# Performance work log

Hardware: AMD Instinct MI355X
Metric: run time of the kernel (lower is better)

## Reference

```python
import jax, jax.numpy as jnp
import numpy as np

B, N, D_IN, D_OUT = 64, 512, 128, 128
LEAKY_SLOPE = 0.2  # DGL GATConv default negative_slope


def setup_inputs() -> dict:
    key = jax.random.key(0)
    k1, k2, k3, k4, k5 = jax.random.split(key, 5)
    embedding = jax.random.normal(k1, (B, N, D_IN), dtype=jnp.float32)
    W = jax.random.normal(k2, (D_IN, D_OUT), dtype=jnp.float32) / np.sqrt(D_IN)
    attn_l = jax.random.normal(k3, (D_OUT,), dtype=jnp.float32) * 0.1
    attn_r = jax.random.normal(k4, (D_OUT,), dtype=jnp.float32) * 0.1
    bias = jax.random.normal(k5, (D_OUT,), dtype=jnp.float32) * 0.01
    return {"embedding": embedding, "W": W, "attn_l": attn_l, "attn_r": attn_r, "bias": bias}


def reference(embedding, W, attn_l, attn_r, bias):
    # --- constructure_graph: per-sample adjacency E @ E^T thresholded at its
    # scalar mean, plus self-loops. edge (i, j): src=i (row), dst=j (col).
    scores = jnp.einsum('bnd,bmd->bnm', embedding, embedding)        # [B,N,N]
    thresh = jnp.mean(scores, axis=(1, 2), keepdims=True)            # scalar per sample
    self_loop = jnp.eye(scores.shape[1], dtype=bool)                  # [N,N]
    mask = (scores > thresh) | self_loop                              # [B,src,dst]

    # --- GATConv (1 head, eval mode: feat_drop/attn_drop are identity)
    z = jnp.einsum('bnd,de->bne', embedding, W)                       # [B,N,D_OUT]
    el = z @ attn_l                                                   # [B,N] source term
    er = z @ attn_r                                                   # [B,N] dest term
    e = jax.nn.leaky_relu(el[:, :, None] + er[:, None, :], LEAKY_SLOPE)  # [B,src,dst]
    e = jnp.where(mask, e, -jnp.inf)
    alpha = jax.nn.softmax(e, axis=1)                                 # softmax over incoming (src) edges per dst
    h = jnp.einsum('bij,bid->bjd', alpha, z)                          # aggregate src -> dst
    h = jax.nn.elu(h + bias)                                          # bias + activation=F.elu

    # --- mean pool over nodes
    return jnp.mean(h, axis=1)                                        # [B, D_OUT]
```

## Files before the change

kernel.cpp:

```cpp
#include <hip/hip_runtime.h>
#include <math.h>

#define BATCH 64
#define NN 512
#define DD 128
#define SLOPE 0.2f

typedef unsigned short u16;
typedef short bf16x8 __attribute__((ext_vector_type(8)));
typedef u16 u16x4 __attribute__((ext_vector_type(4)));
typedef u16 u16x8 __attribute__((ext_vector_type(8)));
typedef float f32x4 __attribute__((ext_vector_type(4)));

static __device__ __forceinline__ u16 f2bf(float x) {
    unsigned int u = __float_as_uint(x);
    return (u16)((u + 0x7fffu + ((u >> 16) & 1u)) >> 16);
}
static __device__ __forceinline__ float bf2f(u16 h) {
    return __uint_as_float(((unsigned int)h) << 16);
}
static __device__ __forceinline__ void gld16(const u16* g, u16* lds) {
    __builtin_amdgcn_global_load_lds(
        (const __attribute__((address_space(1))) unsigned int*)g,
        (__attribute__((address_space(3))) unsigned int*)lds, 16, 0, 0);
}

__global__ __launch_bounds__(256) void k_prep(const float* __restrict__ W,
                                              const float* __restrict__ E,
                                              u16* __restrict__ WtHi,
                                              u16* __restrict__ WtLo,
                                              float* __restrict__ cs2,
                                              float* __restrict__ out) {
    __shared__ float csr[8][128];
    int t = threadIdx.x;
    if (blockIdx.x == 0) {
        int n = t & 127, half = t >> 7;
        #pragma unroll
        for (int g = 0; g < 8; ++g) {
            u16x8 hv, lv;
            #pragma unroll
            for (int j = 0; j < 8; ++j) {
                float v = W[(size_t)(half * 64 + g * 8 + j) * DD + n];
                u16 h = f2bf(v);
                hv[j] = h;
                lv[j] = f2bf(v - bf2f(h));
            }
            *(u16x8*)&WtHi[(size_t)n * DD + half * 64 + g * 8] = hv;
            *(u16x8*)&WtLo[(size_t)n * DD + half * 64 + g * 8] = lv;
        }
    } else {
        int b = (blockIdx.x - 1) >> 1;
        int half = (blockIdx.x - 1) & 1;
        int c4 = t & 31, r0 = t >> 5;
        const float* Eb = E + ((size_t)b * NN + half * 256) * DD;
        float cp0 = 0.f, cp1 = 0.f, cp2 = 0.f, cp3 = 0.f;
        for (int k = 0; k < 32; ++k) {
            int row = r0 + k * 8;
            float4 v = *(const float4*)&Eb[(size_t)row * DD + c4 * 4];
            cp0 += v.x; cp1 += v.y; cp2 += v.z; cp3 += v.w;
        }
        csr[r0][c4 * 4 + 0] = cp0;
        csr[r0][c4 * 4 + 1] = cp1;
        csr[r0][c4 * 4 + 2] = cp2;
        csr[r0][c4 * 4 + 3] = cp3;
        if (t < 64) out[b * DD + half * 64 + t] = 0.f;
        __syncthreads();
        if (t < 128) {
            float s = 0.f;
            #pragma unroll
            for (int g = 0; g < 8; ++g) s += csr[g][t];
            cs2[(size_t)half * BATCH * DD + b * DD + t] = s;
        }
    }
}

__global__ __launch_bounds__(256) void k_z(const float* __restrict__ E,
                                           const u16* __restrict__ WtHi,
                                           const u16* __restrict__ WtLo,
                                           const float* __restrict__ al,
                                           const float* __restrict__ ar,
                                           u16* __restrict__ Ebf,
                                           u16* __restrict__ zT,
                                           float* __restrict__ el,
                                           float* __restrict__ er) {
    int bid = blockIdx.x;
    int b = (bid & 7) * 8 + (bid >> 6);
    int rg = (bid >> 3) & 7;
    int t = threadIdx.x;
    int w = t >> 6;
    int lane = t & 63;
    int l15 = lane & 15;
    int quad = lane >> 4;
    int sg = w >> 1;
    int ch = w & 1;

    __shared__ float elp_s[64], erp_s[64];
    if (t < 64) { elp_s[t] = 0.f; erp_s[t] = 0.f; }
    __syncthreads();

    bf16x8 bh[4][4], bl[4][4];
    float a_l[4], a_r[4];
    #pragma unroll
    for (int c = 0; c < 4; ++c) {
        int nt = ch * 4 + c;
        #pragma unroll
        for (int ks = 0; ks < 4; ++ks) {
            bh[c][ks] = *(const bf16x8*)(WtHi + (size_t)(nt * 16 + l15) * DD + ks * 32 + quad * 8);
            bl[c][ks] = *(const bf16x8*)(WtLo + (size_t)(nt * 16 + l15) * DD + ks * 32 + quad * 8);
        }
        a_l[c] = al[nt * 16 + l15];
        a_r[c] = ar[nt * 16 + l15];
    }

    #pragma unroll
    for (int si = 0; si < 2; ++si) {
        int s = sg * 2 + si;
        int row = rg * 64 + s * 16 + l15;
        const float* Er = E + ((size_t)b * NN + row) * DD;

        bf16x8 ah[4], alo[4];
        #pragma unroll
        for (int ks = 0; ks < 4; ++ks) {
            float4 v0 = *(const float4*)(Er + ks * 32 + quad * 8);
            float4 v1 = *(const float4*)(Er + ks * 32 + quad * 8 + 4);
            float vv[8] = {v0.x, v0.y, v0.z, v0.w, v1.x, v1.y, v1.z, v1.w};
            u16x8 hv, lv;
            #pragma unroll
            for (int j = 0; j < 8; ++j) {
                u16 h = f2bf(vv[j]);
                hv[j] = h;
                lv[j] = f2bf(vv[j] - bf2f(h));
            }
            ah[ks] = (bf16x8)hv;
            alo[ks] = (bf16x8)lv;
            if (ch == 0)
                *(u16x8*)&Ebf[((size_t)b * NN + row) * DD + ks * 32 + quad * 8] = hv;
        }

        f32x4 C[4];
        #pragma unroll
        for (int c = 0; c < 4; ++c) C[c] = (f32x4){0.f, 0.f, 0.f, 0.f};
        #pragma unroll
        for (int ks = 0; ks < 4; ++ks)
            #pragma unroll
            for (int c = 0; c < 4; ++c) {
                C[c] = __builtin_amdgcn_mfma_f32_16x16x32_bf16(ah[ks],  bh[c][ks], C[c], 0, 0, 0);
                C[c] = __builtin_amdgcn_mfma_f32_16x16x32_bf16(alo[ks], bh[c][ks], C[c], 0, 0, 0);
                C[c] = __builtin_amdgcn_mfma_f32_16x16x32_bf16(ah[ks],  bl[c][ks], C[c], 0, 0, 0);
            }

        float elp[4] = {0.f, 0.f, 0.f, 0.f};
        float erp[4] = {0.f, 0.f, 0.f, 0.f};
        #pragma unroll
        for (int c = 0; c < 4; ++c) {
            u16x4 zp;
            #pragma unroll
            for (int r = 0; r < 4; ++r) {
                zp[r] = f2bf(C[c][r]);
                elp[r] += C[c][r] * a_l[c];
                erp[r] += C[c][r] * a_r[c];
            }
            *(u16x4*)&zT[((size_t)b * DD + (ch * 4 + c) * 16 + l15) * NN
                         + rg * 64 + s * 16 + quad * 4] = zp;
        }
        #pragma unroll
        for (int r = 0; r < 4; ++r) {
            float vl = elp[r], vr = erp[r];
            #pragma unroll
            for (int off = 8; off > 0; off >>= 1) {
                vl += __shfl_down(vl, off);
                vr += __shfl_down(vr, off);
            }
            if (l15 == 0) {
                atomicAdd(&elp_s[s * 16 + quad * 4 + r], vl);
                atomicAdd(&erp_s[s * 16 + quad * 4 + r], vr);
            }
        }
    }
    __syncthreads();
    if (t < 64) {
        el[b * NN + rg * 64 + t] = elp_s[t];
        er[b * NN + rg * 64 + t] = erp_s[t];
    }
}

__global__ __launch_bounds__(256, 3) void k_main(const u16* __restrict__ Ebf,
                                                 const u16* __restrict__ zT,
                                                 const float* __restrict__ el,
                                                 const float* __restrict__ er,
                                                 const float* __restrict__ cs2,
                                                 const float* __restrict__ bias,
                                                 float* __restrict__ out) {
    int bid = blockIdx.x;
    int b = (bid & 7) * 8 + (bid >> 6);
    int j0 = ((bid >> 3) & 7) * 64;
    int t = threadIdx.x;
    int w = t >> 6;
    int lane = t & 63;
    int l15 = lane & 15;
    int quad = lane >> 4;
    int jb = j0 + w * 16;

    const u16* Eb = Ebf + (size_t)b * NN * DD;
    const u16* zTb = zT + (size_t)b * DD * NN;

    __shared__ u16 Ei[64 * DD];
    __shared__ u16 zTile[DD * 64];
    __shared__ u16 pT[4][16][72];
    __shared__ float tred[2];

    if (t < 128) {
        float c = cs2[b * DD + t] + cs2[BATCH * DD + b * DD + t];
        float v = c * c;
        #pragma unroll
        for (int off = 32; off > 0; off >>= 1) v += __shfl_down(v, off);
        if ((t & 63) == 0) tred[t >> 6] = v;
    }

    bf16x8 bEj[4];
    #pragma unroll
    for (int ks = 0; ks < 4; ++ks)
        bEj[ks] = *(const bf16x8*)(Eb + (size_t)(jb + l15) * DD + ks * 32 + quad * 8);
    float er_v = er[b * NN + jb + l15];

    f32x4 H[8];
    #pragma unroll
    for (int nt = 0; nt < 8; ++nt) H[nt] = (f32x4){0.f, 0.f, 0.f, 0.f};
    f32x4 CZ = (f32x4){0.f, 0.f, 0.f, 0.f};
    bf16x8 one8;
    #pragma unroll
    for (int j = 0; j < 8; ++j) one8[j] = (short)0x3F80;

    __syncthreads();
    float thr = (tred[0] + tred[1]) * (1.0f / ((float)NN * (float)NN));

    int eswz = l15 & 7;

    for (int c = 0; c < 8; ++c) {
        int i0 = c * 64;

        #pragma unroll
        for (int g = 0; g < 4; ++g) {
            int rloc = w * 16 + g * 4 + (lane >> 4);
            int pcb = lane & 15;
            const u16* gp = Eb + (size_t)(i0 + rloc) * DD + (pcb ^ (rloc & 7)) * 8;
            gld16(gp, &Ei[(w * 16 + g * 4) * DD]);
        }
        #pragma unroll
        for (int g = 0; g < 4; ++g) {
            int dloc = w * 32 + g * 8 + (lane >> 3);
            int pcb = lane & 7;
            const u16* gp = zTb + (size_t)dloc * NN + i0 + (pcb ^ (dloc & 7)) * 8;
            gld16(gp, &zTile[(w * 32 + g * 8) * 64]);
        }
        __syncthreads();

        #pragma unroll
        for (int it = 0; it < 4; ++it) {
            bf16x8 aE[4];
            #pragma unroll
            for (int ks = 0; ks < 4; ++ks)
                aE[ks] = *(const bf16x8*)&Ei[(it * 16 + l15) * DD + ((ks * 4 + quad) ^ eswz) * 8];
            f32x4 S = (f32x4){0.f, 0.f, 0.f, 0.f};
            #pragma unroll
            for (int ks = 0; ks < 4; ++ks)
                S = __builtin_amdgcn_mfma_f32_16x16x32_bf16(aE[ks], bEj[ks], S, 0, 0, 0);

            float4 el4 = *(const float4*)(el + b * NN + i0 + it * 16 + quad * 4);
            float elv[4] = {el4.x, el4.y, el4.z, el4.w};
            u16x4 pk;
            if (i0 + it * 16 == jb) {
                #pragma unroll
                for (int r = 0; r < 4; ++r) {
                    float x = elv[r] + er_v;
                    float lg = x > 0.f ? x : SLOPE * x;
                    bool keep = (S[r] > thr) || ((quad * 4 + r) == l15);
                    pk[r] = f2bf(keep ? __expf(lg) : 0.f);
                }
            } else {
                #pragma unroll
                for (int r = 0; r < 4; ++r) {
                    float x = elv[r] + er_v;
                    float lg = x > 0.f ? x : SLOPE * x;
                    pk[r] = f2bf((S[r] > thr) ? __expf(lg) : 0.f);
                }
            }
            *(u16x4*)&pT[w][l15][it * 16 + quad * 4] = pk;
        }

        bf16x8 ap[2];
        #pragma unroll
        for (int ks = 0; ks < 2; ++ks)
            ap[ks] = *(const bf16x8*)&pT[w][l15][ks * 32 + quad * 8];

        #pragma unroll
        for (int ks = 0; ks < 2; ++ks) {
            CZ = __builtin_amdgcn_mfma_f32_16x16x32_bf16(ap[ks], one8, CZ, 0, 0, 0);
            #pragma unroll
            for (int nt = 0; nt < 8; ++nt) {
                bf16x8 bz = *(const bf16x8*)&zTile[(nt * 16 + l15) * 64 + ((ks * 4 + quad) ^ eswz) * 8];
                H[nt] = __builtin_amdgcn_mfma_f32_16x16x32_bf16(ap[ks], bz, H[nt], 0, 0, 0);
            }
        }
        __syncthreads();
    }

    float zinv[4];
    #pragma unroll
    for (int r = 0; r < 4; ++r) zinv[r] = 1.0f / CZ[r];

    #pragma unroll
    for (int nt = 0; nt < 8; ++nt) {
        float bsv = bias[nt * 16 + l15];
        float acc = 0.f;
        #pragma unroll
        for (int r = 0; r < 4; ++r) {
            float v = H[nt][r] * zinv[r] + bsv;
            v = v > 0.f ? v : (__expf(v) - 1.f);
            acc += v;
        }
        acc += __shfl_down(acc, 32);
        acc += __shfl_down(acc, 16);
        if (lane < 16) atomicAdd(&out[b * DD + nt * 16 + lane], acc * (1.0f / NN));
    }
}

extern "C" void kernel_launch(void* const* d_in, const int* in_sizes, int n_in,
                              void* d_out, int out_size, void* d_ws, size_t ws_size,
                              hipStream_t stream) {
    const float* E    = (const float*)d_in[0];
    const float* W    = (const float*)d_in[1];
    const float* al   = (const float*)d_in[2];
    const float* ar   = (const float*)d_in[3];
    const float* bias = (const float*)d_in[4];
    float* out = (float*)d_out;

    u16* Ebf = (u16*)d_ws;
    u16* zTb = Ebf + (size_t)BATCH * NN * DD;
    u16* WtHi = zTb + (size_t)BATCH * NN * DD;
    u16* WtLo = WtHi + (size_t)DD * DD;
    float* el  = (float*)(WtLo + (size_t)DD * DD);
    float* er  = el + (size_t)BATCH * NN;
    float* cs2 = er + (size_t)BATCH * NN;

    k_prep<<<dim3(129), dim3(256), 0, stream>>>(W, E, WtHi, WtLo, cs2, out);
    k_z<<<dim3(512), dim3(256), 0, stream>>>(E, WtHi, WtLo, al, ar, Ebf, zTb, el, er);
    k_main<<<dim3(512), dim3(256), 0, stream>>>(Ebf, zTb, el, er, cs2, bias, out);
}
```

Baseline: 121.2 us.

## Fold prep kernel into k_z and restructure k_main to direct-register tiles

Removes the separate prep kernel: each k_z block now converts its W slice to hi/lo bf16 itself, accumulates column sums of E as it loads rows, and zeroes the output. k_main is reorganised so each wave owns 16 source rows against all 64 destination columns. It loads E and zT tiles straight from global into registers instead of staging them through LDS with async copies. The softmax denominator is now accumulated in scalar code from the bf16-rounded weights instead of through an extra MFMA against ones. This saves a launch and LDS traffic, but adds redundant W conversion in every k_z block and more global reads and register pressure (launch bound lowered to 2 blocks per unit).

Measured after the change: 121.1 us. No clear change (-0.0%).

```diff
diff --git a/kernel.cpp b/kernel.cpp
--- a/kernel.cpp
+++ b/kernel.cpp
@@ -19,70 +19,17 @@
 static __device__ __forceinline__ float bf2f(u16 h) {
     return __uint_as_float(((unsigned int)h) << 16);
 }
-static __device__ __forceinline__ void gld16(const u16* g, u16* lds) {
-    __builtin_amdgcn_global_load_lds(
-        (const __attribute__((address_space(1))) unsigned int*)g,
-        (__attribute__((address_space(3))) unsigned int*)lds, 16, 0, 0);
-}
-
-__global__ __launch_bounds__(256) void k_prep(const float* __restrict__ W,
-                                              const float* __restrict__ E,
-                                              u16* __restrict__ WtHi,
-                                              u16* __restrict__ WtLo,
-                                              float* __restrict__ cs2,
-                                              float* __restrict__ out) {
-    __shared__ float csr[8][128];
-    int t = threadIdx.x;
-    if (blockIdx.x == 0) {
-        int n = t & 127, half = t >> 7;
-        #pragma unroll
-        for (int g = 0; g < 8; ++g) {
-            u16x8 hv, lv;
-            #pragma unroll
-            for (int j = 0; j < 8; ++j) {
-                float v = W[(size_t)(half * 64 + g * 8 + j) * DD + n];
-                u16 h = f2bf(v);
-                hv[j] = h;
-                lv[j] = f2bf(v - bf2f(h));
-            }
-            *(u16x8*)&WtHi[(size_t)n * DD + half * 64 + g * 8] = hv;
-            *(u16x8*)&WtLo[(size_t)n * DD + half * 64 + g * 8] = lv;
-        }
-    } else {
-        int b = (blockIdx.x - 1) >> 1;
-        int half = (blockIdx.x - 1) & 1;
-        int c4 = t & 31, r0 = t >> 5;
-        const float* Eb = E + ((size_t)b * NN + half * 256) * DD;
-        float cp0 = 0.f, cp1 = 0.f, cp2 = 0.f, cp3 = 0.f;
-        for (int k = 0; k < 32; ++k) {
-            int row = r0 + k * 8;
-            float4 v = *(const float4*)&Eb[(size_t)row * DD + c4 * 4];
-            cp0 += v.x; cp1 += v.y; cp2 += v.z; cp3 += v.w;
-        }
-        csr[r0][c4 * 4 + 0] = cp0;
-        csr[r0][c4 * 4 + 1] = cp1;
-        csr[r0][c4 * 4 + 2] = cp2;
-        csr[r0][c4 * 4 + 3] = cp3;
-        if (t < 64) out[b * DD + half * 64 + t] = 0.f;
-        __syncthreads();
-        if (t < 128) {
-            float s = 0.f;
-            #pragma unroll
-            for (int g = 0; g < 8; ++g) s += csr[g][t];
-            cs2[(size_t)half * BATCH * DD + b * DD + t] = s;
-        }
-    }
-}
 
 __global__ __launch_bounds__(256) void k_z(const float* __restrict__ E,
-                                           const u16* __restrict__ WtHi,
-                                           const u16* __restrict__ WtLo,
+                                           const float* __restrict__ W,
                                            const float* __restrict__ al,
                                            const float* __restrict__ ar,
                                            u16* __restrict__ Ebf,
                                            u16* __restrict__ zT,
                                            float* __restrict__ el,
-                                           float* __restrict__ er) {
+                                           float* __restrict__ er,
+                                           float* __restrict__ cs8,
+                                           float* __restrict__ out) {
     int bid = blockIdx.x;
     int b = (bid & 7) * 8 + (bid >> 6);
     int rg = (bid >> 3) & 7;
@@ -95,22 +42,36 @@
     int ch = w & 1;
 
     __shared__ float elp_s[64], erp_s[64];
+    __shared__ float csp[2][128];
     if (t < 64) { elp_s[t] = 0.f; erp_s[t] = 0.f; }
+    if (rg == 0 && t < 128) out[b * DD + t] = 0.f;
     __syncthreads();
 
     bf16x8 bh[4][4], bl[4][4];
     float a_l[4], a_r[4];
     #pragma unroll
     for (int c = 0; c < 4; ++c) {
-        int nt = ch * 4 + c;
+        int n = (ch * 4 + c) * 16 + l15;
         #pragma unroll
         for (int ks = 0; ks < 4; ++ks) {
-            bh[c][ks] = *(const bf16x8*)(WtHi + (size_t)(nt * 16 + l15) * DD + ks * 32 + quad * 8);
-            bl[c][ks] = *(const bf16x8*)(WtLo + (size_t)(nt * 16 + l15) * DD + ks * 32 + quad * 8);
-        }
-        a_l[c] = al[nt * 16 + l15];
-        a_r[c] = ar[nt * 16 + l15];
-    }
+            u16x8 hv, lv;
+            #pragma unroll
+            for (int j = 0; j < 8; ++j) {
+                float v = W[(size_t)(ks * 32 + quad * 8 + j) * DD + n];
+                u16 h = f2bf(v);
+                hv[j] = h;
+                lv[j] = f2bf(v - bf2f(h));
+            }
+            bh[c][ks] = (bf16x8)hv;
+            bl[c][ks] = (bf16x8)lv;
+        }
+        a_l[c] = al[n];
+        a_r[c] = ar[n];
+    }
+
+    float cs_l[32];
+    #pragma unroll
+    for (int i = 0; i < 32; ++i) cs_l[i] = 0.f;
 
     #pragma unroll
     for (int si = 0; si < 2; ++si) {
@@ -130,6 +91,7 @@
                 u16 h = f2bf(vv[j]);
                 hv[j] = h;
                 lv[j] = f2bf(vv[j] - bf2f(h));
+                if (ch == 0) cs_l[ks * 8 + j] += vv[j];
             }
             ah[ks] = (bf16x8)hv;
             alo[ks] = (bf16x8)lv;
@@ -177,18 +139,34 @@
             }
         }
     }
+
+    if (ch == 0) {
+        #pragma unroll
+        for (int ks = 0; ks < 4; ++ks)
+            #pragma unroll
+            for (int j = 0; j < 8; ++j) {
+                float v = cs_l[ks * 8 + j];
+                v += __shfl_down(v, 8);
+                v += __shfl_down(v, 4);
+                v += __shfl_down(v, 2);
+                v += __shfl_down(v, 1);
+                if (l15 == 0) csp[sg][ks * 32 + quad * 8 + j] = v;
+            }
+    }
     __syncthreads();
     if (t < 64) {
         el[b * NN + rg * 64 + t] = elp_s[t];
         er[b * NN + rg * 64 + t] = erp_s[t];
     }
-}
-
-__global__ __launch_bounds__(256, 3) void k_main(const u16* __restrict__ Ebf,
+    if (t < 128)
+        cs8[((size_t)rg * BATCH + b) * DD + t] = csp[0][t] + csp[1][t];
+}
+
+__global__ __launch_bounds__(256, 2) void k_main(const u16* __restrict__ Ebf,
                                                  const u16* __restrict__ zT,
                                                  const float* __restrict__ el,
                                                  const float* __restrict__ er,
-                                                 const float* __restrict__ cs2,
+                                                 const float* __restrict__ cs8,
                                                  const float* __restrict__ bias,
                                                  float* __restrict__ out) {
     int bid = blockIdx.x;
@@ -199,129 +177,144 @@
     int lane = t & 63;
     int l15 = lane & 15;
     int quad = lane >> 4;
-    int jb = j0 + w * 16;
 
     const u16* Eb = Ebf + (size_t)b * NN * DD;
     const u16* zTb = zT + (size_t)b * DD * NN;
 
-    __shared__ u16 Ei[64 * DD];
-    __shared__ u16 zTile[DD * 64];
-    __shared__ u16 pT[4][16][72];
+    __shared__ u16 pT[64][72];
+    __shared__ float zs_part[4][64];
+    __shared__ float zfin[64];
     __shared__ float tred[2];
 
     if (t < 128) {
-        float c = cs2[b * DD + t] + cs2[BATCH * DD + b * DD + t];
-        float v = c * c;
+        float cc = 0.f;
+        #pragma unroll
+        for (int rg = 0; rg < 8; ++rg)
+            cc += cs8[((size_t)rg * BATCH + b) * DD + t];
+        float v = cc * cc;
         #pragma unroll
         for (int off = 32; off > 0; off >>= 1) v += __shfl_down(v, off);
         if ((t & 63) == 0) tred[t >> 6] = v;
     }
 
-    bf16x8 bEj[4];
-    #pragma unroll
-    for (int ks = 0; ks < 4; ++ks)
-        bEj[ks] = *(const bf16x8*)(Eb + (size_t)(jb + l15) * DD + ks * 32 + quad * 8);
-    float er_v = er[b * NN + jb + l15];
-
-    f32x4 H[8];
-    #pragma unroll
-    for (int nt = 0; nt < 8; ++nt) H[nt] = (f32x4){0.f, 0.f, 0.f, 0.f};
-    f32x4 CZ = (f32x4){0.f, 0.f, 0.f, 0.f};
-    bf16x8 one8;
-    #pragma unroll
-    for (int j = 0; j < 8; ++j) one8[j] = (short)0x3F80;
+    bf16x8 bEj[4][4];
+    #pragma unroll
+    for (int jt = 0; jt < 4; ++jt)
+        #pragma unroll
+        for (int ks = 0; ks < 4; ++ks)
+            bEj[jt][ks] = *(const bf16x8*)(Eb + (size_t)(j0 + jt * 16 + l15) * DD + ks * 32 + quad * 8);
+    float er_v[4];
+    #pragma unroll
+    for (int jt = 0; jt < 4; ++jt) er_v[jt] = er[b * NN + j0 + jt * 16 + l15];
+    float bsv[2] = { bias[(2 * w + 0) * 16 + l15], bias[(2 * w + 1) * 16 + l15] };
+
+    f32x4 H[4][2];
+    #pragma unroll
+    for (int jt = 0; jt < 4; ++jt) {
+        H[jt][0] = (f32x4){0.f, 0.f, 0.f, 0.f};
+        H[jt][1] = (f32x4){0.f, 0.f, 0.f, 0.f};
+    }
+    float zp[4] = {0.f, 0.f, 0.f, 0.f};
 
     __syncthreads();
     float thr = (tred[0] + tred[1]) * (1.0f / ((float)NN * (float)NN));
 
-    int eswz = l15 & 7;
-
-    for (int c = 0; c < 8; ++c) {
-        int i0 = c * 64;
-
-        #pragma unroll
-        for (int g = 0; g < 4; ++g) {
-            int rloc = w * 16 + g * 4 + (lane >> 4);
-            int pcb = lane & 15;
-            const u16* gp = Eb + (size_t)(i0 + rloc) * DD + (pcb ^ (rloc & 7)) * 8;
-            gld16(gp, &Ei[(w * 16 + g * 4) * DD]);
-        }
-        #pragma unroll
-        for (int g = 0; g < 4; ++g) {
-            int dloc = w * 32 + g * 8 + (lane >> 3);
-            int pcb = lane & 7;
-            const u16* gp = zTb + (size_t)dloc * NN + i0 + (pcb ^ (dloc & 7)) * 8;
-            gld16(gp, &zTile[(w * 32 + g * 8) * 64]);
+    for (int c8 = 0; c8 < 8; ++c8) {
+        int i0 = c8 * 64;
+
+        bf16x8 bz[2][2];
+        #pragma unroll
+        for (int cc = 0; cc < 2; ++cc)
+            #pragma unroll
+            for (int ks = 0; ks < 2; ++ks)
+                bz[cc][ks] = *(const bf16x8*)(zTb + (size_t)((2 * w + cc) * 16 + l15) * NN + i0 + ks * 32 + quad * 8);
+
+        bf16x8 aE[4];
+        #pragma unroll
+        for (int ks = 0; ks < 4; ++ks)
+            aE[ks] = *(const bf16x8*)(Eb + (size_t)(i0 + w * 16 + l15) * DD + ks * 32 + quad * 8);
+        float4 el4 = *(const float4*)(el + b * NN + i0 + w * 16 + quad * 4);
+
+        f32x4 S[4];
+        #pragma unroll
+        for (int jt = 0; jt < 4; ++jt) S[jt] = (f32x4){0.f, 0.f, 0.f, 0.f};
+        #pragma unroll
+        for (int ks = 0; ks < 4; ++ks)
+            #pragma unroll
+            for (int jt = 0; jt < 4; ++jt)
+                S[jt] = __builtin_amdgcn_mfma_f32_16x16x32_bf16(aE[ks], bEj[jt][ks], S[jt], 0, 0, 0);
+
+        float elv[4] = {el4.x, el4.y, el4.z, el4.w};
+        int ig_base = i0 + w * 16 + quad * 4;
+        #pragma unroll
+        for (int jt = 0; jt < 4; ++jt) {
+            int jg = j0 + jt * 16 + l15;
+            float erv = er_v[jt];
+            float ls = 0.f;
+            u16x4 pk;
+            #pragma unroll
+            for (int r = 0; r < 4; ++r) {
+                float x = elv[r] + erv;
+                float lg = x > 0.f ? x : SLOPE * x;
+                bool keep = (S[jt][r] > thr) || (ig_base + r == jg);
+                float pe = keep ? __expf(lg) : 0.f;
+                u16 pb = f2bf(pe);
+                pk[r] = pb;
+                ls += bf2f(pb);
+            }
+            zp[jt] += ls;
+            *(u16x4*)&pT[jt * 16 + l15][w * 16 + quad * 4] = pk;
         }
         __syncthreads();
 
         #pragma unroll
-        for (int it = 0; it < 4; ++it) {
-            bf16x8 aE[4];
-            #pragma unroll
-            for (int ks = 0; ks < 4; ++ks)
-                aE[ks] = *(const bf16x8*)&Ei[(it * 16 + l15) * DD + ((ks * 4 + quad) ^ eswz) * 8];
-            f32x4 S = (f32x4){0.f, 0.f, 0.f, 0.f};
-            #pragma unroll
-            for (int ks = 0; ks < 4; ++ks)
-                S = __builtin_amdgcn_mfma_f32_16x16x32_bf16(aE[ks], bEj[ks], S, 0, 0, 0);
-
-            float4 el4 = *(const float4*)(el + b * NN + i0 + it * 16 + quad * 4);
-            float elv[4] = {el4.x, el4.y, el4.z, el4.w};
-            u16x4 pk;
-            if (i0 + it * 16 == jb) {
+        for (int jt = 0; jt < 4; ++jt) {
+            bf16x8 ap[2];
+            #pragma unroll
+            for (int ks = 0; ks < 2; ++ks)
+                ap[ks] = *(const bf16x8*)&pT[jt * 16 + l15][ks * 32 + quad * 8];
+            #pragma unroll
+            for (int ks = 0; ks < 2; ++ks)
                 #pragma unroll
-                for (int r = 0; r < 4; ++r) {
-                    float x = elv[r] + er_v;
-                    float lg = x > 0.f ? x : SLOPE * x;
-                    bool keep = (S[r] > thr) || ((quad * 4 + r) == l15);
-                    pk[r] = f2bf(keep ? __expf(lg) : 0.f);
-                }
-            } else {
-                #pragma unroll
-                for (int r = 0; r < 4; ++r) {
-                    float x = elv[r] + er_v;
-                    float lg = x > 0.f ? x : SLOPE * x;
-                    pk[r] = f2bf((S[r] > thr) ? __expf(lg) : 0.f);
-                }
-            }
-            *(u16x4*)&pT[w][l15][it * 16 + quad * 4] = pk;
-        }
-
-        bf16x8 ap[2];
-        #pragma unroll
-        for (int ks = 0; ks < 2; ++ks)
-            ap[ks] = *(const bf16x8*)&pT[w][l15][ks * 32 + quad * 8];
-
-        #pragma unroll
-        for (int ks = 0; ks < 2; ++ks) {
-            CZ = __builtin_amdgcn_mfma_f32_16x16x32_bf16(ap[ks], one8, CZ, 0, 0, 0);
-            #pragma unroll
-            for (int nt = 0; nt < 8; ++nt) {
-                bf16x8 bz = *(const bf16x8*)&zTile[(nt * 16 + l15) * 64 + ((ks * 4 + quad) ^ eswz) * 8];
-                H[nt] = __builtin_amdgcn_mfma_f32_16x16x32_bf16(ap[ks], bz, H[nt], 0, 0, 0);
-            }
+                for (int cc = 0; cc < 2; ++cc)
+                    H[jt][cc] = __builtin_amdgcn_mfma_f32_16x16x32_bf16(ap[ks], bz[cc][ks], H[jt][cc], 0, 0, 0);
         }
         __syncthreads();
     }
 
-    float zinv[4];
-    #pragma unroll
-    for (int r = 0; r < 4; ++r) zinv[r] = 1.0f / CZ[r];
-
-    #pragma unroll
-    for (int nt = 0; nt < 8; ++nt) {
-        float bsv = bias[nt * 16 + l15];
-        float acc = 0.f;
-        #pragma unroll
-        for (int r = 0; r < 4; ++r) {
-            float v = H[nt][r] * zinv[r] + bsv;
-            v = v > 0.f ? v : (__expf(v) - 1.f);
-            acc += v;
-        }
-        acc += __shfl_down(acc, 32);
-        acc += __shfl_down(acc, 16);
-        if (lane < 16) atomicAdd(&out[b * DD + nt * 16 + lane], acc * (1.0f / NN));
+    #pragma unroll
+    for (int jt = 0; jt < 4; ++jt) {
+        float v = zp[jt];
+        v += __shfl_down(v, 32);
+        v += __shfl_down(v, 16);
+        if (lane < 16) zs_part[w][jt * 16 + lane] = v;
+    }
+    __syncthreads();
+    if (t < 64)
+        zfin[t] = 1.0f / (zs_part[0][t] + zs_part[1][t] + zs_part[2][t] + zs_part[3][t]);
+    __syncthreads();
+
+    float acc[2] = {0.f, 0.f};
+    #pragma unroll
+    for (int jt = 0; jt < 4; ++jt) {
+        float4 zi = *(const float4*)&zfin[jt * 16 + quad * 4];
+        float ziv[4] = {zi.x, zi.y, zi.z, zi.w};
+        #pragma unroll
+        for (int cc = 0; cc < 2; ++cc)
+            #pragma unroll
+            for (int r = 0; r < 4; ++r) {
+                float v = H[jt][cc][r] * ziv[r] + bsv[cc];
+                v = v > 0.f ? v : (__expf(v) - 1.f);
+                acc[cc] += v;
+            }
+    }
+    #pragma unroll
+    for (int cc = 0; cc < 2; ++cc) {
+        float v = acc[cc];
+        v += __shfl_down(v, 32);
+        v += __shfl_down(v, 16);
+        if (lane < 16)
+            atomicAdd(&out[b * DD + (2 * w + cc) * 16 + lane], v * (1.0f / NN));
     }
 }
 
@@ -337,13 +330,10 @@
 
     u16* Ebf = (u16*)d_ws;
     u16* zTb = Ebf + (size_t)BATCH * NN * DD;
-    u16* WtHi = zTb + (size_t)BATCH * NN * DD;
-    u16* WtLo = WtHi + (size_t)DD * DD;
-    float* el  = (float*)(WtLo + (size_t)DD * DD);
+    float* el  = (float*)(zTb + (size_t)BATCH * NN * DD);
     float* er  = el + (size_t)BATCH * NN;
-    float* cs2 = er + (size_t)BATCH * NN;
-
-    k_prep<<<dim3(129), dim3(256), 0, stream>>>(W, E, WtHi, WtLo, cs2, out);
-    k_z<<<dim3(512), dim3(256), 0, stream>>>(E, WtHi, WtLo, al, ar, Ebf, zTb, el, er);
-    k_main<<<dim3(512), dim3(256), 0, stream>>>(Ebf, zTb, el, er, cs2, bias, out);
-}
+    float* cs8 = er + (size_t)BATCH * NN;
+
+    k_z<<<dim3(512), dim3(256), 0, stream>>>(E, W, al, ar, Ebf, zTb, el, er, cs8, out);
+    k_main<<<dim3(512), dim3(256), 0, stream>>>(Ebf, zTb, el, er, cs8, bias, out);
+}
```
